# Kernel optimization log

Hardware: AMD Instinct MI355X
Metric: run time of the kernel (lower is better)

## Reference

```python
import jax, jax.numpy as jnp
import numpy as np
import math

B, S, D, H, WD = 8, 2048, 512, 8, 64
DK = D // H


def setup_inputs() -> dict:
    k = jax.random.key(0)
    ks = jax.random.split(k, 16)
    s = 0.02
    return {
        "query": jax.random.normal(ks[0], (B, S, D), jnp.float32),
        "key": jax.random.normal(ks[1], (B, S, D), jnp.float32),
        "value": jax.random.normal(ks[2], (B, S, D), jnp.float32),
        "mask": jax.random.randint(ks[3], (B, S), 0, 2, jnp.int32),
        "segment_weights": jax.random.uniform(ks[4], (B, S, S), jnp.float32),
        # torch Linear weights: [out_features, in_features]
        "Wq": jax.random.normal(ks[5], (D, D), jnp.float32) * s,
        "bq": jnp.zeros((D,), jnp.float32),
        "Wk": jax.random.normal(ks[6], (D, D), jnp.float32) * s,
        "bk": jnp.zeros((D,), jnp.float32),
        "Wv": jax.random.normal(ks[7], (D, D), jnp.float32) * s,
        "bv": jnp.zeros((D,), jnp.float32),
        "Wo": jax.random.normal(ks[8], (D, D), jnp.float32) * s,
        "bo": jnp.zeros((D,), jnp.float32),
        "Wl": jax.random.normal(ks[9], (WD, 1), jnp.float32) * 0.1,
        "bl": jnp.zeros((WD,), jnp.float32),
        "Wr": jax.random.normal(ks[10], (1, WD), jnp.float32) * 0.1,
        "br": jnp.zeros((1,), jnp.float32),
    }


def reference(query, key, value, mask, segment_weights,
              Wq, bq, Wk, bk, Wv, bv, Wo, bo, Wl, bl, Wr, br):
    nb = query.shape[0]
    # segment bias MLP: 1 -> WD -> 1 with leaky_relu(0.2)
    sw = 1.0 / jnp.log(jnp.float32(math.e) + segment_weights)  # [B,S,S]
    hmid = jax.nn.leaky_relu(sw[..., None] * Wl[:, 0] + bl, negative_slope=0.2)  # [B,S,S,WD]
    bias = (hmid @ Wr.T + br)[..., 0]  # [B,S,S]

    def proj(x, W, b):
        return (x @ W.T + b).reshape(nb, -1, H, DK).transpose(0, 2, 1, 3)  # [B,H,S,DK]

    q = proj(query, Wq, bq)
    k = proj(key, Wk, bk)
    v = proj(value, Wv, bv)

    scores = jnp.einsum("bhqd,bhkd->bhqk", q, k) / jnp.float32(math.sqrt(DK))
    scores = scores + bias[:, None]  # broadcast over heads
    # mask [B,S] -> [B,1,S,1]: masks query rows (as in original)
    scores = jnp.where(mask[:, None, :, None] == 0, jnp.float32(-1e9), scores)
    p = jax.nn.softmax(scores, axis=-1)
    x = jnp.einsum("bhqk,bhkd->bhqd", p, v)
    x = x.transpose(0, 2, 1, 3).reshape(nb, -1, H * DK)
    return x @ Wo.T + bo
```

## Files before the change

kernel.cpp:

```cpp
#include <hip/hip_runtime.h>
#include <stdint.h>

#define Bb 8
#define Ss 2048
#define Dd 512
#define Hh 8

typedef unsigned short u16;
typedef __attribute__((ext_vector_type(8))) short s16x8;
typedef __attribute__((ext_vector_type(4))) unsigned short u16x4;
typedef __attribute__((ext_vector_type(4))) float f32x4;

__device__ __forceinline__ u16 f2bf(float f){
  unsigned u = __float_as_uint(f);
  return (u16)((u + 0x7fffu + ((u>>16)&1u)) >> 16);
}

__device__ __forceinline__ void gl_lds16(const void* g, void* l){
  __builtin_amdgcn_global_load_lds((const __attribute__((address_space(1))) unsigned int*)g,
                                   (__attribute__((address_space(3))) unsigned int*)l, 16, 0, 0);
}

#define MFMA32(a,b,c) __builtin_amdgcn_mfma_f32_16x16x32_bf16(a,b,c,0,0,0)

__global__ __launch_bounds__(256) void castw(const float* __restrict__ a, const float* __restrict__ b,
                                             const float* __restrict__ c, const float* __restrict__ d,
                                             u16* __restrict__ o){
  int i = blockIdx.x*256 + threadIdx.x;
  const float* src = (i < 65536) ? a : (i < 131072) ? b : (i < 196608) ? c : d;
  int off = (i & 65535) << 2;
  f32x4 v = *(const f32x4*)(src + off);
  u16x4 r;
  #pragma unroll
  for(int j = 0; j < 4; j++) r[j] = f2bf(v[j]);
  *(u16x4*)(o + ((size_t)(i >> 16) << 18) + off) = r;
}

__global__ void prep(const float* __restrict__ Wl, const float* __restrict__ bl,
                     const float* __restrict__ Wr, const float* __restrict__ br,
                     float* __restrict__ consts){
  int w = threadIdx.x;
  float wl = Wl[w], blv = bl[w], wr = Wr[w];
  float h0 = 0.75f*wl + blv; h0 = h0 > 0.f ? h0 : 0.2f*h0;
  float h1 = 1.00f*wl + blv; h1 = h1 > 0.f ? h1 : 0.2f*h1;
  float f0 = wr*h0, f1 = wr*h1;
  #pragma unroll
  for(int off = 32; off > 0; off >>= 1){
    f0 += __shfl_down(f0, off);
    f1 += __shfl_down(f1, off);
  }
  if(w == 0){
    float brv = br[0];
    float F0 = f0 + brv, F1 = f1 + brv;
    float C1 = (F1 - F0) * 4.0f;
    float C0 = F0 - 0.75f*C1;
    consts[0] = C1 * 1.4426950408889634f;
    consts[1] = C0;
  }
}

template<int MODE>
__global__ __launch_bounds__(256) void gemm_t(const void* __restrict__ Ap, const u16* __restrict__ W,
                                              const float* __restrict__ bias, void* __restrict__ Cp){
  __shared__ __align__(16) u16 As[128*32];
  __shared__ __align__(16) u16 Bs[128*32];
  const int t = threadIdx.x;
  const int lane = t & 63, wv = t >> 6;
  const int quad = lane >> 4, l15 = lane & 15;
  const int m0 = blockIdx.x * 128, n0 = blockIdx.y * 128;
  const int R = (wv >> 1) * 64, Cc = (wv & 1) * 64;
  f32x4 acc[4][4] = {};
  for(int kb = 0; kb < 512; kb += 32){
    __syncthreads();
    #pragma unroll
    for(int i = 0; i < 2; i++){
      int u  = i*256 + t;
      int m  = u >> 2;
      int cc = (u & 3) ^ ((m >> 1) & 3);
      if (MODE == 2){
        gl_lds16((const u16*)Ap + (size_t)(m0 + m)*512 + kb + cc*8, As + (size_t)(i*256 + wv*64)*8);
      } else {
        const float* src = (const float*)Ap + (size_t)(m0 + m)*512 + kb + cc*8;
        f32x4 v0 = *(const f32x4*)src;
        f32x4 v1 = *(const f32x4*)(src + 4);
        s16x8 cv;
        #pragma unroll
        for(int r2 = 0; r2 < 4; r2++){ cv[r2] = (short)f2bf(v0[r2]); cv[4+r2] = (short)f2bf(v1[r2]); }
        *(s16x8*)(As + (size_t)u*8) = cv;
      }
      gl_lds16(W + (size_t)(n0 + m)*512 + kb + cc*8, Bs + (size_t)(i*256 + wv*64)*8);
    }
    __syncthreads();
    s16x8 af[4], bfr[4];
    #pragma unroll
    for(int mi = 0; mi < 4; mi++){
      int m = R + mi*16 + l15;
      int u = (m << 2) | (quad ^ ((m >> 1) & 3));
      af[mi] = *(const s16x8*)(As + (size_t)u*8);
    }
    #pragma unroll
    for(int ni = 0; ni < 4; ni++){
      int n = Cc + ni*16 + l15;
      int u = (n << 2) | (quad ^ ((n >> 1) & 3));
      bfr[ni] = *(const s16x8*)(Bs + (size_t)u*8);
    }
    #pragma unroll
    for(int mi = 0; mi < 4; mi++)
      #pragma unroll
      for(int ni = 0; ni < 4; ni++)
        acc[mi][ni] = MFMA32(af[mi], bfr[ni], acc[mi][ni]);
  }
  #pragma unroll
  for(int ni = 0; ni < 4; ni++){
    int col = n0 + Cc + ni*16 + l15;
    float bv = bias[col];
    #pragma unroll
    for(int mi = 0; mi < 4; mi++){
      int row0 = m0 + R + mi*16 + quad*4;
      #pragma unroll
      for(int r = 0; r < 4; r++){
        float v = acc[mi][ni][r] + bv;
        int row = row0 + r;
        if (MODE == 2)      ((float*)Cp)[(size_t)row*512 + col] = v;
        else if (MODE == 1) ((u16*)Cp)[(size_t)((row >> 11)*512 + col)*2048 + (size_t)(row & 2047)] = f2bf(v);
        else                ((u16*)Cp)[(size_t)row*512 + col] = f2bf(v);
      }
    }
  }
}

__global__ __launch_bounds__(512, 2) void attn(const u16* __restrict__ qp, const u16* __restrict__ kp,
                                               const u16* __restrict__ vt, const float* __restrict__ seg,
                                               const int* __restrict__ mask, const float* __restrict__ consts,
                                               u16* __restrict__ xo){
  __shared__ __align__(16) float bias_s[64*36];
  const int t = threadIdx.x;
  const int lane = t & 63, h = t >> 6;
  const int quad = lane >> 4, l15 = lane & 15;
  const int b = blockIdx.x >> 5, q0 = (blockIdx.x & 31) * 64;
  const float C1 = consts[0], C0 = consts[1];
  const int krA = 8*(l15 >> 2) + (l15 & 3);

  s16x8 qf[4][2];
  #pragma unroll
  for(int ni = 0; ni < 4; ni++){
    const u16* qrow = qp + (size_t)(b*Ss + q0 + ni*16 + l15)*Dd + h*64;
    qf[ni][0] = *(const s16x8*)(qrow + quad*8);
    qf[ni][1] = *(const s16x8*)(qrow + 32 + quad*8);
  }
  float mk[4];
  #pragma unroll
  for(int ni = 0; ni < 4; ni++)
    mk[ni] = (mask[b*Ss + q0 + ni*16 + l15] == 0) ? 0.0f : 1.0f;

  f32x4 ot[4][4] = {};
  float lsum[4] = {0.f, 0.f, 0.f, 0.f};

  const int sq = t >> 3, sk = (t & 7) * 4;
  const float* segrow = seg + ((size_t)b*Ss + (size_t)(q0 + sq))*Ss + sk;

  for(int k0 = 0; k0 < Ss; k0 += 32){
    __syncthreads();
    {
      f32x4 raw = *(const f32x4*)(segrow + k0);
      f32x4 bv;
      #pragma unroll
      for(int j = 0; j < 4; j++){
        float x = 2.718281828459045f + raw[j];
        bv[j] = C1 * __builtin_amdgcn_rcpf(__log2f(x)) + C0;
      }
      *(f32x4*)(bias_s + sq*36 + sk) = bv;
    }
    __syncthreads();

    f32x4 st[2][4] = {};
    #pragma unroll
    for(int ks = 0; ks < 2; ks++){
      s16x8 kf[2];
      #pragma unroll
      for(int mi = 0; mi < 2; mi++)
        kf[mi] = *(const s16x8*)(kp + (size_t)(b*Ss + k0 + krA + mi*4)*Dd + h*64 + ks*32 + quad*8);
      #pragma unroll
      for(int mi = 0; mi < 2; mi++)
        #pragma unroll
        for(int ni = 0; ni < 4; ni++)
          st[mi][ni] = MFMA32(kf[mi], qf[ni][ks], st[mi][ni]);
    }

    s16x8 pf8[4];
    #pragma unroll
    for(int mi = 0; mi < 2; mi++)
      #pragma unroll
      for(int ni = 0; ni < 4; ni++){
        f32x4 bb = *(const f32x4*)(bias_s + (ni*16 + l15)*36 + quad*8 + mi*4);
        f32x4 s = st[mi][ni] * 0.125f + bb;
        s *= mk[ni];
        #pragma unroll
        for(int r = 0; r < 4; r++){
          float sv = fminf(fmaxf(s[r], -30.f), 30.f);
          float p = __expf(sv);
          lsum[ni] += p;
          pf8[ni][mi*4 + r] = (short)f2bf(p);
        }
      }

    #pragma unroll
    for(int mi2 = 0; mi2 < 4; mi2++){
      s16x8 vf = *(const s16x8*)(vt + (size_t)(b*Dd + h*64 + mi2*16 + l15)*Ss + k0 + quad*8);
      #pragma unroll
      for(int ni = 0; ni < 4; ni++)
        ot[mi2][ni] = MFMA32(vf, pf8[ni], ot[mi2][ni]);
    }
  }

  float rl[4];
  #pragma unroll
  for(int ni = 0; ni < 4; ni++){
    float l = lsum[ni];
    l += __shfl_xor(l, 16);
    l += __shfl_xor(l, 32);
    rl[ni] = 1.0f / l;
  }

  #pragma unroll
  for(int ni = 0; ni < 4; ni++)
    #pragma unroll
    for(int mi2 = 0; mi2 < 4; mi2++){
      u16x4 o;
      #pragma unroll
      for(int r = 0; r < 4; r++) o[r] = f2bf(ot[mi2][ni][r] * rl[ni]);
      *(u16x4*)(xo + (size_t)(b*Ss + q0 + ni*16 + l15)*Dd + h*64 + mi2*16 + quad*4) = o;
    }
}

extern "C" void kernel_launch(void* const* d_in, const int* in_sizes, int n_in,
                              void* d_out, int out_size, void* d_ws, size_t ws_size,
                              hipStream_t stream){
  const float* query = (const float*)d_in[0];
  const float* key   = (const float*)d_in[1];
  const float* value = (const float*)d_in[2];
  const int*   mask  = (const int*)d_in[3];
  const float* seg   = (const float*)d_in[4];
  const float* Wq = (const float*)d_in[5];  const float* bq = (const float*)d_in[6];
  const float* Wk = (const float*)d_in[7];  const float* bk = (const float*)d_in[8];
  const float* Wv = (const float*)d_in[9];  const float* bv = (const float*)d_in[10];
  const float* Wo = (const float*)d_in[11]; const float* bo = (const float*)d_in[12];
  const float* Wl = (const float*)d_in[13]; const float* bl = (const float*)d_in[14];
  const float* Wr = (const float*)d_in[15]; const float* br = (const float*)d_in[16];

  char* ws = (char*)d_ws;
  float* consts = (float*)ws;
  u16* Wc  = (u16*)(ws + 4096);
  u16* qp  = (u16*)(ws + ((size_t)4  << 20));
  u16* kp  = (u16*)(ws + ((size_t)20 << 20));
  u16* vt  = (u16*)(ws + ((size_t)36 << 20));
  u16* xo  = qp;
  const size_t WN = (size_t)512*512;

  castw<<<1024, 256, 0, stream>>>(Wq, Wk, Wv, Wo, Wc);
  prep<<<1, 64, 0, stream>>>(Wl, bl, Wr, br, consts);
  gemm_t<0><<<dim3(128,4), 256, 0, stream>>>(query, Wc + 0*WN, bq, qp);
  gemm_t<0><<<dim3(128,4), 256, 0, stream>>>(key,   Wc + 1*WN, bk, kp);
  gemm_t<1><<<dim3(128,4), 256, 0, stream>>>(value, Wc + 2*WN, bv, vt);
  attn<<<256, 512, 0, stream>>>(qp, kp, vt, seg, mask, consts, xo);
  gemm_t<2><<<dim3(128,4), 256, 0, stream>>>(xo, Wc + 3*WN, bo, d_out);
}
```

Measured before the change: 552.4 us.

## Merge QKV GEMMs, halve attention query tile, use exp2 with bit-pack bf16

Merges the three projection GEMMs into one launch indexed by blockIdx.z, and register-prefetches the next fp32 activation tile while converting the current one. The attention query tile drops from 64 to 32 rows, doubling the grid to 512 blocks with occupancy hint 4. Only half the threads now compute the segment bias. Softmax moves to exp2 with log2e folded into the bias constants and the score scale, drops the clamp, accumulates row sums as vectors, and packs bf16 with perm (round-half-up instead of round-to-even). Smaller tiles re-read K and V more often and the unclamped exp could overflow, in exchange for more parallelism and cheaper per-element math.

```diff
diff --git a/kernel.cpp b/kernel.cpp
--- a/kernel.cpp
+++ b/kernel.cpp
@@ -9,6 +9,7 @@
 typedef unsigned short u16;
 typedef __attribute__((ext_vector_type(8))) short s16x8;
 typedef __attribute__((ext_vector_type(4))) unsigned short u16x4;
+typedef __attribute__((ext_vector_type(4))) unsigned int u32x4;
 typedef __attribute__((ext_vector_type(4))) float f32x4;
 
 __device__ __forceinline__ u16 f2bf(float f){
@@ -54,14 +55,103 @@
     float F0 = f0 + brv, F1 = f1 + brv;
     float C1 = (F1 - F0) * 4.0f;
     float C0 = F0 - 0.75f*C1;
-    consts[0] = C1 * 1.4426950408889634f;
-    consts[1] = C0;
-  }
-}
-
-template<int MODE>
-__global__ __launch_bounds__(256) void gemm_t(const void* __restrict__ Ap, const u16* __restrict__ W,
-                                              const float* __restrict__ bias, void* __restrict__ Cp){
+    consts[0] = C1 * 2.0813689810056077f;
+    consts[1] = C0 * 1.4426950408889634f;
+  }
+}
+
+__global__ __launch_bounds__(256) void qkv_gemm(const float* __restrict__ Aq, const float* __restrict__ Ak,
+                                                const float* __restrict__ Av, const u16* __restrict__ Wc,
+                                                const float* __restrict__ bq, const float* __restrict__ bk,
+                                                const float* __restrict__ bv,
+                                                u16* __restrict__ oq, u16* __restrict__ ok2, u16* __restrict__ ov){
+  __shared__ __align__(16) u16 As[128*32];
+  __shared__ __align__(16) u16 Bs[128*32];
+  const int z = blockIdx.z;
+  const float* A    = (z == 0) ? Aq : (z == 1) ? Ak : Av;
+  const float* bias = (z == 0) ? bq : (z == 1) ? bk : bv;
+  const u16* W = Wc + (size_t)z * 512 * 512;
+  const int t = threadIdx.x;
+  const int lane = t & 63, wv = t >> 6;
+  const int quad = lane >> 4, l15 = lane & 15;
+  const int m0 = blockIdx.x * 128, n0 = blockIdx.y * 128;
+  const int R = (wv >> 1) * 64, Cc = (wv & 1) * 64;
+
+  int mm[2], uu[2], cc8[2];
+  #pragma unroll
+  for(int i = 0; i < 2; i++){
+    int u = i*256 + t;
+    int m = u >> 2;
+    int cc = (u & 3) ^ ((m >> 1) & 3);
+    mm[i] = m; uu[i] = u; cc8[i] = cc*8;
+  }
+  f32x4 pa[2][2];
+  #pragma unroll
+  for(int i = 0; i < 2; i++){
+    const float* src = A + (size_t)(m0 + mm[i])*512 + cc8[i];
+    pa[i][0] = *(const f32x4*)src;
+    pa[i][1] = *(const f32x4*)(src + 4);
+  }
+
+  f32x4 acc[4][4] = {};
+  for(int kb = 0; kb < 512; kb += 32){
+    __syncthreads();
+    #pragma unroll
+    for(int i = 0; i < 2; i++){
+      s16x8 cv;
+      #pragma unroll
+      for(int r2 = 0; r2 < 4; r2++){ cv[r2] = (short)f2bf(pa[i][0][r2]); cv[4+r2] = (short)f2bf(pa[i][1][r2]); }
+      *(s16x8*)(As + (size_t)uu[i]*8) = cv;
+      gl_lds16(W + (size_t)(n0 + mm[i])*512 + kb + cc8[i], Bs + (size_t)(i*256 + wv*64)*8);
+    }
+    if (kb + 32 < 512){
+      #pragma unroll
+      for(int i = 0; i < 2; i++){
+        const float* src = A + (size_t)(m0 + mm[i])*512 + kb + 32 + cc8[i];
+        pa[i][0] = *(const f32x4*)src;
+        pa[i][1] = *(const f32x4*)(src + 4);
+      }
+    }
+    __syncthreads();
+    s16x8 af[4], bfr[4];
+    #pragma unroll
+    for(int mi = 0; mi < 4; mi++){
+      int m = R + mi*16 + l15;
+      int u = (m << 2) | (quad ^ ((m >> 1) & 3));
+      af[mi] = *(const s16x8*)(As + (size_t)u*8);
+    }
+    #pragma unroll
+    for(int ni = 0; ni < 4; ni++){
+      int n = Cc + ni*16 + l15;
+      int u = (n << 2) | (quad ^ ((n >> 1) & 3));
+      bfr[ni] = *(const s16x8*)(Bs + (size_t)u*8);
+    }
+    #pragma unroll
+    for(int mi = 0; mi < 4; mi++)
+      #pragma unroll
+      for(int ni = 0; ni < 4; ni++)
+        acc[mi][ni] = MFMA32(af[mi], bfr[ni], acc[mi][ni]);
+  }
+  #pragma unroll
+  for(int ni = 0; ni < 4; ni++){
+    int col = n0 + Cc + ni*16 + l15;
+    float bv2 = bias[col];
+    #pragma unroll
+    for(int mi = 0; mi < 4; mi++){
+      int row0 = m0 + R + mi*16 + quad*4;
+      #pragma unroll
+      for(int r = 0; r < 4; r++){
+        float v = acc[mi][ni][r] + bv2;
+        int row = row0 + r;
+        if (z == 2) ov[(size_t)((row >> 11)*512 + col)*2048 + (size_t)(row & 2047)] = f2bf(v);
+        else        ((z == 0) ? oq : ok2)[(size_t)row*512 + col] = f2bf(v);
+      }
+    }
+  }
+}
+
+__global__ __launch_bounds__(256) void gemm_o(const u16* __restrict__ A, const u16* __restrict__ W,
+                                              const float* __restrict__ bias, float* __restrict__ C){
   __shared__ __align__(16) u16 As[128*32];
   __shared__ __align__(16) u16 Bs[128*32];
   const int t = threadIdx.x;
@@ -77,17 +167,7 @@
       int u  = i*256 + t;
       int m  = u >> 2;
       int cc = (u & 3) ^ ((m >> 1) & 3);
-      if (MODE == 2){
-        gl_lds16((const u16*)Ap + (size_t)(m0 + m)*512 + kb + cc*8, As + (size_t)(i*256 + wv*64)*8);
-      } else {
-        const float* src = (const float*)Ap + (size_t)(m0 + m)*512 + kb + cc*8;
-        f32x4 v0 = *(const f32x4*)src;
-        f32x4 v1 = *(const f32x4*)(src + 4);
-        s16x8 cv;
-        #pragma unroll
-        for(int r2 = 0; r2 < 4; r2++){ cv[r2] = (short)f2bf(v0[r2]); cv[4+r2] = (short)f2bf(v1[r2]); }
-        *(s16x8*)(As + (size_t)u*8) = cv;
-      }
+      gl_lds16(A + (size_t)(m0 + m)*512 + kb + cc*8, As + (size_t)(i*256 + wv*64)*8);
       gl_lds16(W + (size_t)(n0 + m)*512 + kb + cc*8, Bs + (size_t)(i*256 + wv*64)*8);
     }
     __syncthreads();
@@ -118,62 +198,57 @@
     for(int mi = 0; mi < 4; mi++){
       int row0 = m0 + R + mi*16 + quad*4;
       #pragma unroll
-      for(int r = 0; r < 4; r++){
-        float v = acc[mi][ni][r] + bv;
-        int row = row0 + r;
-        if (MODE == 2)      ((float*)Cp)[(size_t)row*512 + col] = v;
-        else if (MODE == 1) ((u16*)Cp)[(size_t)((row >> 11)*512 + col)*2048 + (size_t)(row & 2047)] = f2bf(v);
-        else                ((u16*)Cp)[(size_t)row*512 + col] = f2bf(v);
-      }
-    }
-  }
-}
-
-__global__ __launch_bounds__(512, 2) void attn(const u16* __restrict__ qp, const u16* __restrict__ kp,
+      for(int r = 0; r < 4; r++)
+        C[(size_t)(row0 + r)*512 + col] = acc[mi][ni][r] + bv;
+    }
+  }
+}
+
+__global__ __launch_bounds__(512, 4) void attn(const u16* __restrict__ qp, const u16* __restrict__ kp,
                                                const u16* __restrict__ vt, const float* __restrict__ seg,
                                                const int* __restrict__ mask, const float* __restrict__ consts,
                                                u16* __restrict__ xo){
-  __shared__ __align__(16) float bias_s[64*36];
+  __shared__ __align__(16) float bias_s[32*36];
   const int t = threadIdx.x;
   const int lane = t & 63, h = t >> 6;
   const int quad = lane >> 4, l15 = lane & 15;
-  const int b = blockIdx.x >> 5, q0 = (blockIdx.x & 31) * 64;
-  const float C1 = consts[0], C0 = consts[1];
+  const int b = blockIdx.x >> 6, q0 = (blockIdx.x & 63) * 32;
+  const float Cb1 = consts[0], Cb0 = consts[1];
   const int krA = 8*(l15 >> 2) + (l15 & 3);
 
-  s16x8 qf[4][2];
-  #pragma unroll
-  for(int ni = 0; ni < 4; ni++){
+  s16x8 qf[2][2];
+  #pragma unroll
+  for(int ni = 0; ni < 2; ni++){
     const u16* qrow = qp + (size_t)(b*Ss + q0 + ni*16 + l15)*Dd + h*64;
     qf[ni][0] = *(const s16x8*)(qrow + quad*8);
     qf[ni][1] = *(const s16x8*)(qrow + 32 + quad*8);
   }
-  float mk[4];
-  #pragma unroll
-  for(int ni = 0; ni < 4; ni++)
+  float mk[2];
+  #pragma unroll
+  for(int ni = 0; ni < 2; ni++)
     mk[ni] = (mask[b*Ss + q0 + ni*16 + l15] == 0) ? 0.0f : 1.0f;
 
-  f32x4 ot[4][4] = {};
-  float lsum[4] = {0.f, 0.f, 0.f, 0.f};
+  f32x4 ot[4][2] = {};
+  f32x4 lacc[2] = {};
 
   const int sq = t >> 3, sk = (t & 7) * 4;
   const float* segrow = seg + ((size_t)b*Ss + (size_t)(q0 + sq))*Ss + sk;
 
   for(int k0 = 0; k0 < Ss; k0 += 32){
     __syncthreads();
-    {
+    if (t < 256){
       f32x4 raw = *(const f32x4*)(segrow + k0);
       f32x4 bv;
       #pragma unroll
       for(int j = 0; j < 4; j++){
         float x = 2.718281828459045f + raw[j];
-        bv[j] = C1 * __builtin_amdgcn_rcpf(__log2f(x)) + C0;
+        bv[j] = Cb1 * __builtin_amdgcn_rcpf(__log2f(x)) + Cb0;
       }
       *(f32x4*)(bias_s + sq*36 + sk) = bv;
     }
     __syncthreads();
 
-    f32x4 st[2][4] = {};
+    f32x4 st[2][2] = {};
     #pragma unroll
     for(int ks = 0; ks < 2; ks++){
       s16x8 kf[2];
@@ -183,47 +258,53 @@
       #pragma unroll
       for(int mi = 0; mi < 2; mi++)
         #pragma unroll
-        for(int ni = 0; ni < 4; ni++)
+        for(int ni = 0; ni < 2; ni++)
           st[mi][ni] = MFMA32(kf[mi], qf[ni][ks], st[mi][ni]);
     }
 
-    s16x8 pf8[4];
-    #pragma unroll
-    for(int mi = 0; mi < 2; mi++)
-      #pragma unroll
-      for(int ni = 0; ni < 4; ni++){
+    s16x8 pf8[2];
+    #pragma unroll
+    for(int ni = 0; ni < 2; ni++){
+      u32x4 pk;
+      #pragma unroll
+      for(int mi = 0; mi < 2; mi++){
         f32x4 bb = *(const f32x4*)(bias_s + (ni*16 + l15)*36 + quad*8 + mi*4);
-        f32x4 s = st[mi][ni] * 0.125f + bb;
+        f32x4 s = st[mi][ni] * 0.18033688011112042f + bb;
         s *= mk[ni];
+        f32x4 p;
         #pragma unroll
-        for(int r = 0; r < 4; r++){
-          float sv = fminf(fmaxf(s[r], -30.f), 30.f);
-          float p = __expf(sv);
-          lsum[ni] += p;
-          pf8[ni][mi*4 + r] = (short)f2bf(p);
-        }
+        for(int r = 0; r < 4; r++) p[r] = exp2f(s[r]);
+        lacc[ni] += p;
+        unsigned a0 = __float_as_uint(p[0]) + 0x8000u;
+        unsigned a1 = __float_as_uint(p[1]) + 0x8000u;
+        unsigned a2 = __float_as_uint(p[2]) + 0x8000u;
+        unsigned a3 = __float_as_uint(p[3]) + 0x8000u;
+        pk[mi*2]   = __builtin_amdgcn_perm(a1, a0, 0x07060302u);
+        pk[mi*2+1] = __builtin_amdgcn_perm(a3, a2, 0x07060302u);
       }
+      pf8[ni] = __builtin_bit_cast(s16x8, pk);
+    }
 
     #pragma unroll
     for(int mi2 = 0; mi2 < 4; mi2++){
       s16x8 vf = *(const s16x8*)(vt + (size_t)(b*Dd + h*64 + mi2*16 + l15)*Ss + k0 + quad*8);
       #pragma unroll
-      for(int ni = 0; ni < 4; ni++)
+      for(int ni = 0; ni < 2; ni++)
         ot[mi2][ni] = MFMA32(vf, pf8[ni], ot[mi2][ni]);
     }
   }
 
-  float rl[4];
-  #pragma unroll
-  for(int ni = 0; ni < 4; ni++){
-    float l = lsum[ni];
+  float rl[2];
+  #pragma unroll
+  for(int ni = 0; ni < 2; ni++){
+    float l = (lacc[ni][0] + lacc[ni][1]) + (lacc[ni][2] + lacc[ni][3]);
     l += __shfl_xor(l, 16);
     l += __shfl_xor(l, 32);
     rl[ni] = 1.0f / l;
   }
 
   #pragma unroll
-  for(int ni = 0; ni < 4; ni++)
+  for(int ni = 0; ni < 2; ni++)
     #pragma unroll
     for(int mi2 = 0; mi2 < 4; mi2++){
       u16x4 o;
@@ -241,10 +322,14 @@
   const float* value = (const float*)d_in[2];
   const int*   mask  = (const int*)d_in[3];
   const float* seg   = (const float*)d_in[4];
-  const float* Wq = (const float*)d_in[5];  const float* bq = (const float*)d_in[6];
-  const float* Wk = (const float*)d_in[7];  const float* bk = (const float*)d_in[8];
-  const float* Wv = (const float*)d_in[9];  const float* bv = (const float*)d_in[10];
-  const float* Wo = (const float*)d_in[11]; const float* bo = (const float*)d_in[12];
+  const float* bq = (const float*)d_in[6];
+  const float* bk = (const float*)d_in[8];
+  const float* bv = (const float*)d_in[10];
+  const float* bo = (const float*)d_in[12];
+  const float* Wq = (const float*)d_in[5];
+  const float* Wk = (const float*)d_in[7];
+  const float* Wv = (const float*)d_in[9];
+  const float* Wo = (const float*)d_in[11];
   const float* Wl = (const float*)d_in[13]; const float* bl = (const float*)d_in[14];
   const float* Wr = (const float*)d_in[15]; const float* br = (const float*)d_in[16];
 
@@ -259,9 +344,7 @@
 
   castw<<<1024, 256, 0, stream>>>(Wq, Wk, Wv, Wo, Wc);
   prep<<<1, 64, 0, stream>>>(Wl, bl, Wr, br, consts);
-  gemm_t<0><<<dim3(128,4), 256, 0, stream>>>(query, Wc + 0*WN, bq, qp);
-  gemm_t<0><<<dim3(128,4), 256, 0, stream>>>(key,   Wc + 1*WN, bk, kp);
-  gemm_t<1><<<dim3(128,4), 256, 0, stream>>>(value, Wc + 2*WN, bv, vt);
-  attn<<<256, 512, 0, stream>>>(qp, kp, vt, seg, mask, consts, xo);
-  gemm_t<2><<<dim3(128,4), 256, 0, stream>>>(xo, Wc + 3*WN, bo, d_out);
-}
+  qkv_gemm<<<dim3(128,4,3), 256, 0, stream>>>(query, key, value, Wc, bq, bk, bv, qp, kp, vt);
+  attn<<<512, 512, 0, stream>>>(qp, kp, vt, seg, mask, consts, xo);
+  gemm_o<<<dim3(128,4), 256, 0, stream>>>(xo, Wc + 3*WN, bo, (float*)d_out);
+}
```

Measured after the change: 610.5 us. 10.5% more time.
